# Performance work log

Hardware: AMD Instinct MI355X
Metric: run time of the kernel (lower is better)

The kernel has to match this reference:

```python
import jax, jax.numpy as jnp
import numpy as np

B, S, H, E, V, T = 64, 256, 1024, 512, 10000, 64
D = H // 2  # per-direction LSTM hidden


def setup_inputs() -> dict:
    key = jax.random.key(0)
    ks = jax.random.split(key, 16)
    s = jnp.float32(0.02)
    emb = jax.random.normal(ks[4], (V, E), jnp.float32) * s
    emb = emb.at[0].set(0.0)  # padding_idx=0
    return {
        "encoder_outputs": jax.random.normal(ks[0], (B, S, H), jnp.float32),
        "enc_h0": jax.random.normal(ks[1], (2, B, D), jnp.float32),
        "enc_c0": jax.random.normal(ks[2], (2, B, D), jnp.float32),
        "target": jax.random.randint(ks[3], (B, T), 1, V),
        "mask": jnp.zeros((B, S), jnp.bool_),
        "sos_idx": 1,
        "emb": emb,
        "Wa": jax.random.normal(ks[5], (H, H), jnp.float32) * s,
        "Ua": jax.random.normal(ks[6], (H, H), jnp.float32) * s,
        "Va": jax.random.normal(ks[7], (H,), jnp.float32) * s,
        "out_W": jax.random.normal(ks[8], (V, H), jnp.float32) * s,
        "out_b": jnp.zeros((V,), jnp.float32),
        "Wih_f": jax.random.normal(ks[9], (4 * D, E + H), jnp.float32) * s,
        "Whh_f": jax.random.normal(ks[10], (4 * D, D), jnp.float32) * s,
        "bih_f": jnp.zeros((4 * D,), jnp.float32),
        "bhh_f": jnp.zeros((4 * D,), jnp.float32),
        "Wih_b": jax.random.normal(ks[11], (4 * D, E + H), jnp.float32) * s,
        "Whh_b": jax.random.normal(ks[12], (4 * D, D), jnp.float32) * s,
        "bih_b": jnp.zeros((4 * D,), jnp.float32),
        "bhh_b": jnp.zeros((4 * D,), jnp.float32),
    }


def _lstm_cell(x, h, c, Wih, Whh, bih, bhh):
    g = x @ Wih.T + h @ Whh.T + bih + bhh
    i, f, gg, o = jnp.split(g, 4, axis=-1)  # torch gate order i,f,g,o
    c2 = jax.nn.sigmoid(f) * c + jax.nn.sigmoid(i) * jnp.tanh(gg)
    h2 = jax.nn.sigmoid(o) * jnp.tanh(c2)
    return h2, c2


def reference(encoder_outputs, enc_h0, enc_c0, target, mask, sos_idx, emb, Wa, Ua, Va,
              out_W, out_b, Wih_f, Whh_f, bih_f, bhh_f, Wih_b, Whh_b, bih_b, bhh_b):
    # Cache Ua(keys) once (original recomputes it each step; math identical).
    Uk = jnp.einsum('bsh,kh->bsk', encoder_outputs, Ua)  # [B,S,H]
    b = encoder_outputs.shape[0]
    tokens = jnp.concatenate(
        [jnp.full((b, 1), sos_idx, target.dtype), target[:, :-1]], axis=1)  # [B,T]
    xs = tokens.T  # [T,B]

    def step(carry, tok):
        h, c = carry  # each [2,B,D]
        query = jnp.swapaxes(h, 0, 1).reshape(b, -1)  # [B,H] (fwd||bwd)
        sc = jnp.einsum('bsh,h->bs', jnp.tanh((query @ Wa.T)[:, None, :] + Uk), Va)
        sc = jnp.where(mask, -jnp.inf, sc)
        w = jax.nn.softmax(sc, axis=-1)  # [B,S]
        ctx = jnp.einsum('bs,bsh->bh', w, encoder_outputs)  # [B,H]
        x = jnp.concatenate([emb[tok], ctx], axis=-1)  # [B,E+H]
        hf, cf = _lstm_cell(x, h[0], c[0], Wih_f, Whh_f, bih_f, bhh_f)
        hb, cb = _lstm_cell(x, h[1], c[1], Wih_b, Whh_b, bih_b, bhh_b)
        out = jnp.concatenate([hf, hb], axis=-1)  # [B,H]
        logits = out @ out_W.T + out_b  # [B,V]
        return (jnp.stack([hf, hb]), jnp.stack([cf, cb])), (logits, w)

    (h, c), (logits, attns) = jax.lax.scan(step, (enc_h0, enc_c0), xs)
    decoder_outputs = jnp.swapaxes(logits, 0, 1)  # [B,T,V]
    attentions = jnp.swapaxes(attns, 0, 1)        # [B,T,S]
    return decoder_outputs, h, c, attentions
```

## Files before the change

kernel.cpp:

```cpp
#include <hip/hip_runtime.h>

#define NB 64
#define NS 256
#define NH 1024
#define NE 512
#define NV 10000
#define NT 64
#define ND 512
#define NEH 1536
#define HST (65 * NH)

typedef __attribute__((ext_vector_type(8))) short bf16x8;
typedef __attribute__((ext_vector_type(4))) float f32x4;

__device__ __forceinline__ short F2B(float f) {
  unsigned u = __float_as_uint(f);
  return (short)((u + 0x7fffu + ((u >> 16) & 1u)) >> 16);
}
__device__ __forceinline__ float B2F(short s) {
  return __uint_as_float(((unsigned)(unsigned short)s) << 16);
}
__device__ __forceinline__ float ftanh(float x) {
  float e = __expf(2.f * x);
  return 1.f - 2.f * __builtin_amdgcn_rcpf(e + 1.f);
}

#define GLD16(src, dst)                                                        \
  __builtin_amdgcn_global_load_lds(                                            \
      (const __attribute__((address_space(1))) void*)(src),                    \
      (__attribute__((address_space(3))) void*)(dst), 16, 0, 0)

__device__ __forceinline__ void mm64_f32a(
    const float* __restrict__ Af, int lda, const short* __restrict__ Wg,
    int ldw, int K, short* Ch, size_t ldc, char* smem)
{
  const int tid = threadIdx.x;
  const int lane = tid & 63, w = tid >> 6;
  const int qm = (w >> 1) << 5, qn = (w & 1) << 5;
  const int kg = lane >> 4, rl = lane & 15;
  f32x4 acc[2][2] = {};
  const int nIt = K >> 6;

  auto stage = [&](int k0, int buf) {
    char* As = smem + (buf << 14);
    char* Bs = As + 8192;
#pragma unroll
    for (int p = 0; p < 2; ++p) {
      int j = tid + (p << 8);
      int row = j >> 3;
      int c = (j & 7) ^ (row & 7);
      const float* src = Af + (size_t)row * lda + k0 + (c << 3);
      float4 v0 = ((const float4*)src)[0];
      float4 v1 = ((const float4*)src)[1];
      bf16x8 pk;
      pk[0] = F2B(v0.x); pk[1] = F2B(v0.y); pk[2] = F2B(v0.z); pk[3] = F2B(v0.w);
      pk[4] = F2B(v1.x); pk[5] = F2B(v1.y); pk[6] = F2B(v1.z); pk[7] = F2B(v1.w);
      *((bf16x8*)As + j) = pk;
    }
#pragma unroll
    for (int p = 0; p < 2; ++p) {
      int j = (w << 7) + (p << 6) + lane;
      int row = j >> 3;
      int c = (j & 7) ^ (row & 7);
      GLD16(Wg + (size_t)row * ldw + k0 + (c << 3), Bs + (w << 11) + (p << 10));
    }
  };

  stage(0, 0);
  for (int it = 0; it < nIt; ++it) {
    __syncthreads();
    if (it + 1 < nIt) stage((it + 1) << 6, (it + 1) & 1);
    const short* As = (const short*)(smem + ((it & 1) << 14));
    const short* Bs = As + 4096;
#pragma unroll
    for (int kk = 0; kk < 2; ++kk) {
      bf16x8 af[2], bfr[2];
#pragma unroll
      for (int mt = 0; mt < 2; ++mt) {
        int r2 = qm + (mt << 4) + rl;
        int c = (kk << 2) + kg;
        af[mt] = *((const bf16x8*)As + ((r2 << 3) | (c ^ (r2 & 7))));
      }
#pragma unroll
      for (int nt = 0; nt < 2; ++nt) {
        int r2 = qn + (nt << 4) + rl;
        int c = (kk << 2) + kg;
        bfr[nt] = *((const bf16x8*)Bs + ((r2 << 3) | (c ^ (r2 & 7))));
      }
#pragma unroll
      for (int mt = 0; mt < 2; ++mt)
#pragma unroll
        for (int nt = 0; nt < 2; ++nt)
          acc[mt][nt] = __builtin_amdgcn_mfma_f32_16x16x32_bf16(
              af[mt], bfr[nt], acc[mt][nt], 0, 0, 0);
    }
  }
#pragma unroll
  for (int mt = 0; mt < 2; ++mt)
#pragma unroll
    for (int nt = 0; nt < 2; ++nt) {
      int cn = qn + (nt << 4) + rl;
#pragma unroll
      for (int r = 0; r < 4; ++r) {
        int rowm = qm + (mt << 4) + (kg << 2) + r;
        Ch[(size_t)rowm * ldc + cn] = F2B(acc[mt][nt][r]);
      }
    }
}

__global__ __launch_bounds__(256) void uk_mm_f32(const float* __restrict__ enc,
                                                 const short* __restrict__ Ua_h,
                                                 short* __restrict__ Uk_h) {
  __shared__ char smem[32768];
  mm64_f32a(enc + (size_t)blockIdx.y * 64 * NH, NH,
            Ua_h + (size_t)blockIdx.x * 64 * NH, NH, NH,
            Uk_h + (size_t)blockIdx.y * 64 * NH + blockIdx.x * 64, NH, smem);
}

template <int MODE>
__global__ __launch_bounds__(256) void mm128p(
    const short* __restrict__ A, const short* __restrict__ Bw, int nvmax,
    const float* __restrict__ bias, float* __restrict__ Cf,
    short* __restrict__ Ch)
{
  __shared__ char smem[65536];
  const int tid = threadIdx.x, lane = tid & 63, w = tid >> 6;
  const int m0 = blockIdx.x << 7;
  const int n0 = blockIdx.y << 7;
  const int qm = (w >> 1) << 6, qn = (w & 1) << 6;
  const int kg = lane >> 4, rl = lane & 15;
  f32x4 acc[4][4] = {};

  auto stage = [&](int it, int buf) {
    char* dst = smem + (buf << 15);
    const int k0 = it << 6;
#pragma unroll
    for (int p = 0; p < 4; ++p) {
      int j = (((w << 2) + p) << 6) + lane;
      int row = j >> 3;
      int c = (j & 7) ^ (row & 7);
      int m = m0 + row;
      size_t arow = (MODE == 0) ? ((size_t)(m >> 6) * 65 + (m & 63) + 1)
                                : (size_t)m;
      GLD16(A + arow * NH + k0 + (c << 3), dst + (((w << 2) + p) << 10));
      int vr = n0 + row; if (vr > nvmax - 1) vr = nvmax - 1;
      GLD16(Bw + (size_t)vr * NH + k0 + (c << 3),
            dst + 16384 + (((w << 2) + p) << 10));
    }
  };

  stage(0, 0); stage(1, 1);
  for (int it = 0; it < 16; ++it) {
    if (it < 15) asm volatile("s_waitcnt vmcnt(8)" ::: "memory");
    else         asm volatile("s_waitcnt vmcnt(0)" ::: "memory");
    __builtin_amdgcn_s_barrier();
    __builtin_amdgcn_sched_barrier(0);
    const short* As = (const short*)(smem + ((it & 1) << 15));
    const short* Bs = As + 8192;
#pragma unroll
    for (int kk = 0; kk < 2; ++kk) {
      bf16x8 af[4], bfr[4];
#pragma unroll
      for (int mt = 0; mt < 4; ++mt) {
        int r2 = qm + (mt << 4) + rl;
        int c = (kk << 2) + kg;
        af[mt] = *((const bf16x8*)As + ((r2 << 3) | (c ^ (r2 & 7))));
      }
#pragma unroll
      for (int nt = 0; nt < 4; ++nt) {
        int r2 = qn + (nt << 4) + rl;
        int c = (kk << 2) + kg;
        bfr[nt] = *((const bf16x8*)Bs + ((r2 << 3) | (c ^ (r2 & 7))));
      }
#pragma unroll
      for (int mt = 0; mt < 4; ++mt)
#pragma unroll
        for (int nt = 0; nt < 4; ++nt)
          acc[mt][nt] = __builtin_amdgcn_mfma_f32_16x16x32_bf16(
              af[mt], bfr[nt], acc[mt][nt], 0, 0, 0);
    }
    __builtin_amdgcn_sched_barrier(0);
    __builtin_amdgcn_s_barrier();
    if (it + 2 < 16) stage(it + 2, it & 1);
  }
#pragma unroll
  for (int nt = 0; nt < 4; ++nt) {
    int colv = n0 + qn + (nt << 4) + rl;
    if (colv < nvmax) {
#pragma unroll
      for (int mt = 0; mt < 4; ++mt)
#pragma unroll
        for (int r = 0; r < 4; ++r) {
          int m = m0 + qm + (mt << 4) + (kg << 2) + r;
          if (MODE == 0) {
            Cf[(size_t)m * NV + colv] = acc[mt][nt][r] + bias[colv];
          } else {
            Ch[(size_t)m * NH + colv] = F2B(acc[mt][nt][r]);
          }
        }
    }
  }
}

__global__ __launch_bounds__(256) void gates_v2(
    const short* __restrict__ Xt, const short* __restrict__ hcur,
    const short* __restrict__ Wcomb, const float* __restrict__ bperm,
    const float* __restrict__ cq_old, float* __restrict__ hq_f,
    float* __restrict__ cq_new, short* __restrict__ hnext)
{
  __shared__ char smem[61440];
  const int tid = threadIdx.x, lane = tid & 63, w = tid >> 6;
  const int kg = lane >> 4, rl = lane & 15;
  const int dir = blockIdx.x >> 7, gi = blockIdx.x & 127;
  const int hoff = dir << 9;
  const short* Wbase = Wcomb + (((size_t)(dir << 11) + (gi << 4)) << 11);

  auto stage = [&](int it, int buf) {
    char* dst = smem + buf * 20480;
#pragma unroll
    for (int g = 0; g < 4; ++g) {
      int row = (g << 4) + (w << 2) + kg;
      int c = rl ^ (row & 15);
      int k = (it << 7) + (c << 3);
      const short* src = (k < NEH)
          ? (Xt + (size_t)row * NEH + k)
          : (hcur + (size_t)row * HST + hoff + (k - NEH));
      GLD16(src, dst + (g << 12) + (w << 10));
    }
    {
      int rowB = (w << 2) + kg;
      int cB = rl ^ rowB;
      int kB = (it << 7) + (cB << 3);
      GLD16(Wbase + (size_t)rowB * 2048 + kB, dst + 16384 + (w << 10));
    }
  };

  stage(0, 0); stage(1, 1); stage(2, 2);
  f32x4 acc = {};
  int buf = 0;
  for (int it = 0; it < 16; ++it) {
    if (it < 14)      asm volatile("s_waitcnt vmcnt(10)" ::: "memory");
    else if (it == 14) asm volatile("s_waitcnt vmcnt(5)" ::: "memory");
    else               asm volatile("s_waitcnt vmcnt(0)" ::: "memory");
    __builtin_amdgcn_s_barrier();
    __builtin_amdgcn_sched_barrier(0);
    const short* As = (const short*)(smem + buf * 20480);
    const short* Bs = (const short*)(smem + buf * 20480 + 16384);
    const int rowA = (w << 4) + rl;
#pragma unroll
    for (int kk = 0; kk < 4; ++kk) {
      int chunk = (kk << 2) | kg;
      bf16x8 af = *((const bf16x8*)As + ((rowA << 4) | (chunk ^ (rowA & 15))));
      bf16x8 bf = *((const bf16x8*)Bs + ((rl << 4) | (chunk ^ rl)));
      acc = __builtin_amdgcn_mfma_f32_16x16x32_bf16(af, bf, acc, 0, 0, 0);
    }
    __builtin_amdgcn_sched_barrier(0);
    __builtin_amdgcn_s_barrier();
    if (it + 3 < 16) stage(it + 3, buf);
    buf = (buf == 2) ? 0 : buf + 1;
  }
  float* gacc = (float*)smem;
#pragma unroll
  for (int r = 0; r < 4; ++r)
    gacc[((w << 4) + (kg << 2) + r) * 17 + rl] = acc[r];
  __syncthreads();
  {
    const int b = tid >> 2, j2 = tid & 3;
    const float* bp = bperm + (dir << 11) + (gi << 4) + (j2 << 2);
    const float* gr = gacc + b * 17 + (j2 << 2);
    float gi_ = gr[0] + bp[0];
    float gf_ = gr[1] + bp[1];
    float gg_ = gr[2] + bp[2];
    float go_ = gr[3] + bp[3];
    const int d = ((gi >> 2) << 4) + (((gi << 2) + j2) & 15);
    const int idx = (b << 10) + hoff + d;
    float c0v = cq_old[idx];
    float si = 1.f / (1.f + __expf(-gi_));
    float sf = 1.f / (1.f + __expf(-gf_));
    float so = 1.f / (1.f + __expf(-go_));
    float tg = ftanh(gg_);
    float c2 = sf * c0v + si * tg;
    float h2 = so * ftanh(c2);
    hq_f[idx] = h2;
    cq_new[idx] = c2;
    hnext[(size_t)b * HST + hoff + d] = F2B(h2);
  }
}

__global__ __launch_bounds__(256) void q_mm2(const short* __restrict__ hcur,
                                             const short* __restrict__ Wa_h,
                                             float* __restrict__ q)
{
  __shared__ char smem[61440];
  const int tid = threadIdx.x, lane = tid & 63, w = tid >> 6;
  const int kg = lane >> 4, rl = lane & 15;
  const int n0 = blockIdx.x << 4;
  const short* Wbase = Wa_h + (size_t)n0 * NH;

  auto stage = [&](int it, int buf) {
    char* dst = smem + buf * 20480;
#pragma unroll
    for (int g = 0; g < 4; ++g) {
      int row = (g << 4) + (w << 2) + kg;
      int c = rl ^ (row & 15);
      int k = (it << 7) + (c << 3);
      GLD16(hcur + (size_t)row * HST + k, dst + (g << 12) + (w << 10));
    }
    {
      int rowB = (w << 2) + kg;
      int cB = rl ^ rowB;
      int kB = (it << 7) + (cB << 3);
      GLD16(Wbase + (size_t)rowB * NH + kB, dst + 16384 + (w << 10));
    }
  };

  stage(0, 0); stage(1, 1); stage(2, 2);
  f32x4 acc = {};
  int buf = 0;
  for (int it = 0; it < 8; ++it) {
    if (it < 6)       asm volatile("s_waitcnt vmcnt(10)" ::: "memory");
    else if (it == 6) asm volatile("s_waitcnt vmcnt(5)" ::: "memory");
    else              asm volatile("s_waitcnt vmcnt(0)" ::: "memory");
    __builtin_amdgcn_s_barrier();
    __builtin_amdgcn_sched_barrier(0);
    const short* As = (const short*)(smem + buf * 20480);
    const short* Bs = (const short*)(smem + buf * 20480 + 16384);
    const int rowA = (w << 4) + rl;
#pragma unroll
    for (int kk = 0; kk < 4; ++kk) {
      int chunk = (kk << 2) | kg;
      bf16x8 af = *((const bf16x8*)As + ((rowA << 4) | (chunk ^ (rowA & 15))));
      bf16x8 bf = *((const bf16x8*)Bs + ((rl << 4) | (chunk ^ rl)));
      acc = __builtin_amdgcn_mfma_f32_16x16x32_bf16(af, bf, acc, 0, 0, 0);
    }
    __builtin_amdgcn_sched_barrier(0);
    __builtin_amdgcn_s_barrier();
    if (it + 3 < 8) stage(it + 3, buf);
    buf = (buf == 2) ? 0 : buf + 1;
  }
#pragma unroll
  for (int r = 0; r < 4; ++r)
    q[(size_t)((w << 4) + (kg << 2) + r) * NH + n0 + rl] = acc[r];
}

__global__ __launch_bounds__(256) void f2b_k(const float* __restrict__ in,
                                             short* __restrict__ out, int n4) {
  int i = blockIdx.x * 256 + threadIdx.x;
  const int stride = gridDim.x * 256;
  for (; i < n4; i += stride) {
    float4 v = ((const float4*)in)[i];
    short4 o;
    o.x = F2B(v.x); o.y = F2B(v.y); o.z = F2B(v.z); o.w = F2B(v.w);
    ((short4*)out)[i] = o;
  }
}

__global__ __launch_bounds__(256) void f2b8_k(const float* __restrict__ in,
                                              short* __restrict__ outb,
                                              unsigned* __restrict__ out8,
                                              int n4) {
  int i = blockIdx.x * 256 + threadIdx.x;
  const int stride = gridDim.x * 256;
  for (; i < n4; i += stride) {
    float4 v = ((const float4*)in)[i];
    short4 o;
    o.x = F2B(v.x); o.y = F2B(v.y); o.z = F2B(v.z); o.w = F2B(v.w);
    ((short4*)outb)[i] = o;
    if (out8) {
      int u = __builtin_amdgcn_cvt_pk_fp8_f32(v.x, v.y, 0, false);
      u = __builtin_amdgcn_cvt_pk_fp8_f32(v.z, v.w, u, true);
      out8[i] = (unsigned)u;
    }
  }
}

__global__ __launch_bounds__(256) void f2b2_k(
    const float* __restrict__ in0, short* __restrict__ out0,
    const float* __restrict__ in1, short* __restrict__ out1, int n4each) {
  int i = blockIdx.x * 256 + threadIdx.x;
  const int stride = gridDim.x * 256;
  for (; i < 2 * n4each; i += stride) {
    const float* in = (i < n4each) ? in0 : in1;
    short* out = (i < n4each) ? out0 : out1;
    int j = (i < n4each) ? i : i - n4each;
    float4 v = ((const float4*)in)[j];
    short4 o;
    o.x = F2B(v.x); o.y = F2B(v.y); o.z = F2B(v.z); o.w = F2B(v.w);
    ((short4*)out)[j] = o;
  }
}

__global__ __launch_bounds__(256) void perm_w(
    const float* __restrict__ Wih_f, const float* __restrict__ Whh_f,
    const float* __restrict__ Wih_b, const float* __restrict__ Whh_b,
    const float* __restrict__ bih_f, const float* __restrict__ bhh_f,
    const float* __restrict__ bih_b, const float* __restrict__ bhh_b,
    short* __restrict__ Wcomb, float* __restrict__ bias_perm)
{
  int i = blockIdx.x * 256 + threadIdx.x;
  int k4 = i & 511;
  int np = (i >> 9) & 2047;
  int dir = i >> 20;
  int gate = np & 3, dlo = (np >> 2) & 15, dblk = np >> 6;
  int d = (dblk << 4) + dlo;
  int r = (gate << 9) + d;
  int k = k4 << 2;
  const float* Wih = dir ? Wih_b : Wih_f;
  const float* Whh = dir ? Whh_b : Whh_f;
  float4 v = (k < NEH) ? *(const float4*)(Wih + (size_t)r * NEH + k)
                       : *(const float4*)(Whh + (size_t)r * ND + (k - NEH));
  short4 o;
  o.x = F2B(v.x); o.y = F2B(v.y); o.z = F2B(v.z); o.w = F2B(v.w);
  *(short4*)(Wcomb + ((size_t)((dir << 11) + np) << 11) + k) = o;
  if (k4 == 0) {
    const float* bi = dir ? bih_b : bih_f;
    const float* bh = dir ? bhh_b : bhh_f;
    bias_perm[(dir << 11) + np] = bi[r] + bh[r];
  }
}

__global__ __launch_bounds__(256) void emb_fill(
    const float* __restrict__ emb, const int* __restrict__ target,
    const int* __restrict__ sos, short* __restrict__ Xbuf)
{
  int idx = blockIdx.x * 256 + threadIdx.x;
  int t = idx >> 13;
  int r = idx & 8191;
  int b = r >> 7, e4 = r & 127;
  int tok = (t == 0) ? sos[0] : target[b * NT + t - 1];
  float4 v = *(const float4*)(emb + (size_t)tok * NE + (e4 << 2));
  short4 o;
  o.x = F2B(v.x); o.y = F2B(v.y); o.z = F2B(v.z); o.w = F2B(v.w);
  *(short4*)(Xbuf + (size_t)(t * NB + b) * NEH + (e4 << 2)) = o;
}

__global__ __launch_bounds__(256) void init_state(
    const float* __restrict__ h0, const float* __restrict__ c0,
    float* __restrict__ hq, float* __restrict__ cq, short* __restrict__ H0) {
  int idx = blockIdx.x * 256 + threadIdx.x;
  int b = idx >> 10, dir = (idx >> 9) & 1, d = idx & 511;
  int src = dir * NB * ND + (b << 9) + d;
  float h = h0[src];
  hq[idx] = h;
  cq[idx] = c0[src];
  H0[(size_t)b * HST + (dir << 9) + d] = F2B(h);
}

__global__ __launch_bounds__(256) void final_state(
    const float* __restrict__ hq, const float* __restrict__ cq,
    float* __restrict__ out_h, float* __restrict__ out_c) {
  int idx = blockIdx.x * 256 + threadIdx.x;
  int dir = idx >> 15, r = idx & 32767, b = r >> 9, d = r & 511;
  int src = b * NH + dir * ND + d;
  out_h[idx] = hq[src];
  out_c[idx] = cq[src];
}

__global__ __launch_bounds__(256) void attn_score(
    const float* __restrict__ q, const short* __restrict__ Uk,
    const float* __restrict__ Va, const unsigned char* __restrict__ mask,
    float* __restrict__ sc) {
  __shared__ float qs[NH];
  const int b = blockIdx.x >> 6;
  {
    int t4 = threadIdx.x << 2;
    *(float4*)(qs + t4) = *(const float4*)(q + (size_t)b * NH + t4);
  }
  __syncthreads();
  const int lane = threadIdx.x & 63, wid = threadIdx.x >> 6;
  const int bs = (blockIdx.x << 2) + wid;
  const short* ukp = Uk + (size_t)bs * NH;
  float acc = 0.f;
#pragma unroll
  for (int i = 0; i < 2; ++i) {
    int h = (i << 9) + (lane << 3);
    bf16x8 uv = *(const bf16x8*)(ukp + h);
    float4 q0 = *(const float4*)(qs + h);
    float4 q1 = *(const float4*)(qs + h + 4);
    float4 v0 = *(const float4*)(Va + h);
    float4 v1 = *(const float4*)(Va + h + 4);
    acc += v0.x * ftanh(q0.x + B2F(uv[0]));
    acc += v0.y * ftanh(q0.y + B2F(uv[1]));
    acc += v0.z * ftanh(q0.z + B2F(uv[2]));
    acc += v0.w * ftanh(q0.w + B2F(uv[3]));
    acc += v1.x * ftanh(q1.x + B2F(uv[4]));
    acc += v1.y * ftanh(q1.y + B2F(uv[5]));
    acc += v1.z * ftanh(q1.z + B2F(uv[6]));
    acc += v1.w * ftanh(q1.w + B2F(uv[7]));
  }
#pragma unroll
  for (int o = 32; o; o >>= 1) acc += __shfl_down(acc, o);
  if (lane == 0) sc[bs] = mask[bs] ? -__builtin_inff() : acc;
}

__global__ __launch_bounds__(512) void ctx_soft(
    const float* __restrict__ sc, const unsigned char* __restrict__ enc8,
    const short* __restrict__ enc_h, const float* __restrict__ enc_f,
    int use_8, int use_h,
    short* __restrict__ Xt, float* __restrict__ attn_out, int t) {
  const int tid = threadIdx.x;
  const int b = blockIdx.x >> 2, qh = blockIdx.x & 3;
  __shared__ float red[8];
  __shared__ float ws[NS];
  __shared__ float4 red4[512];
  const int s8 = tid & 255;
  float v = sc[b * NS + s8];
  float m = v;
#pragma unroll
  for (int o = 32; o; o >>= 1) m = fmaxf(m, __shfl_down(m, o));
  if ((tid & 63) == 0) red[tid >> 6] = m;
  __syncthreads();
  m = fmaxf(fmaxf(fmaxf(red[0], red[1]), fmaxf(red[2], red[3])),
            fmaxf(fmaxf(red[4], red[5]), fmaxf(red[6], red[7])));
  float e = __expf(v - m);
  float su = e;
#pragma unroll
  for (int o = 32; o; o >>= 1) su += __shfl_down(su, o);
  __syncthreads();
  if ((tid & 63) == 0) red[tid >> 6] = su;
  __syncthreads();
  su = red[0] + red[1] + red[2] + red[3];
  float wgt = e / su;
  ws[s8] = wgt;
  if (qh == 0 && tid < 256) attn_out[((size_t)b * NT + t) * NS + tid] = wgt;
  __syncthreads();
  const int w8 = tid >> 6, l = tid & 63;
  const int h = (qh << 8) + (l << 2);
  const int s0 = w8 << 5;
  float4 a = make_float4(0.f, 0.f, 0.f, 0.f);
  if (use_8) {
    const unsigned char* ep = enc8 + ((size_t)b * NS + s0) * NH + h;
#pragma unroll 4
    for (int s = 0; s < 32; ++s) {
      int u = *(const int*)(ep + (size_t)s * NH);
      float wv = ws[s0 + s];
      a.x += wv * __builtin_amdgcn_cvt_f32_fp8(u, 0);
      a.y += wv * __builtin_amdgcn_cvt_f32_fp8(u, 1);
      a.z += wv * __builtin_amdgcn_cvt_f32_fp8(u, 2);
      a.w += wv * __builtin_amdgcn_cvt_f32_fp8(u, 3);
    }
  } else if (use_h) {
    const short* ep = enc_h + ((size_t)b * NS + s0) * NH + h;
    for (int s = 0; s < 32; ++s) {
      short4 vv = *(const short4*)(ep + (size_t)s * NH);
      float wv = ws[s0 + s];
      a.x += wv * B2F(vv.x); a.y += wv * B2F(vv.y);
      a.z += wv * B2F(vv.z); a.w += wv * B2F(vv.w);
    }
  } else {
    const float* ep = enc_f + ((size_t)b * NS + s0) * NH + h;
    for (int s = 0; s < 32; ++s) {
      float4 vv = *(const float4*)(ep + (size_t)s * NH);
      float wv = ws[s0 + s];
      a.x += wv * vv.x; a.y += wv * vv.y; a.z += wv * vv.z; a.w += wv * vv.w;
    }
  }
  red4[(w8 << 6) + l] = a;
  __syncthreads();
  if (tid < 64) {
    float sx = 0.f, sy = 0.f, sz = 0.f, sw = 0.f;
#pragma unroll
    for (int k = 0; k < 8; ++k) {
      float4 r = red4[(k << 6) + tid];
      sx += r.x; sy += r.y; sz += r.z; sw += r.w;
    }
    short4 o;
    o.x = F2B(sx); o.y = F2B(sy); o.z = F2B(sz); o.w = F2B(sw);
    *(short4*)(Xt + (size_t)b * NEH + NE + (qh << 8) + (tid << 2)) = o;
  }
}

extern "C" void kernel_launch(void* const* d_in, const int* in_sizes, int n_in,
                              void* d_out, int out_size, void* d_ws, size_t ws_size,
                              hipStream_t stream)
{
  const float* enc    = (const float*)d_in[0];
  const float* h0     = (const float*)d_in[1];
  const float* c0     = (const float*)d_in[2];
  const int*   target = (const int*)d_in[3];
  const unsigned char* mask = (const unsigned char*)d_in[4];
  const int*   sos    = (const int*)d_in[5];
  const float* emb    = (const float*)d_in[6];
  const float* Wa     = (const float*)d_in[7];
  const float* Ua     = (const float*)d_in[8];
  const float* Va     = (const float*)d_in[9];
  const float* out_W  = (const float*)d_in[10];
  const float* out_b  = (const float*)d_in[11];
  const float* Wih_f  = (const float*)d_in[12];
  const float* Whh_f  = (const float*)d_in[13];
  const float* bih_f  = (const float*)d_in[14];
  const float* bhh_f  = (const float*)d_in[15];
  const float* Wih_b  = (const float*)d_in[16];
  const float* Whh_b  = (const float*)d_in[17];
  const float* bih_b  = (const float*)d_in[18];
  const float* bhh_b  = (const float*)d_in[19];

  float* out_dec  = (float*)d_out;
  float* out_h    = out_dec + (size_t)NB * NT * NV;
  float* out_c    = out_h + 2 * NB * ND;
  float* out_attn = out_c + 2 * NB * ND;

  char* base = (char*)d_ws;
  size_t off = 0;
  auto alloc = [&](size_t bytes) -> char* {
    char* p = base + off;
    off += (bytes + 255) & ~(size_t)255;
    return p;
  };
  short* Uk_h  = (short*)alloc((size_t)NB * NS * NH * 2);
  short* ow_h  = (short*)alloc((size_t)NV * NH * 2);
  short* Ua_h  = (short*)alloc((size_t)NH * NH * 2);
  short* Wa_h  = (short*)alloc((size_t)NH * NH * 2);
  short* Wcomb = (short*)alloc((size_t)2 * 2048 * 2048 * 2);
  float* bperm = (float*)alloc((size_t)2 * 2048 * 4);
  float* q     = (float*)alloc((size_t)NB * NH * 4);
  float* sc    = (float*)alloc((size_t)NB * NS * 4);
  short* Xbuf  = (short*)alloc((size_t)NT * NB * NEH * 2);
  float* hq    = (float*)alloc((size_t)NB * NH * 4);
  float* cq    = (float*)alloc((size_t)2 * NB * NH * 4);
  short* Hbuf  = (short*)alloc((size_t)NB * HST * 2);
  short* enc_h = nullptr;
  unsigned char* enc8 = nullptr;
  int use_h = 0, use_8 = 0;
  if (off + (size_t)NB * NS * NH * 2 <= ws_size) {
    enc_h = (short*)alloc((size_t)NB * NS * NH * 2);
    use_h = 1;
    if (off + (size_t)NB * NS * NH <= ws_size) {
      enc8 = (unsigned char*)alloc((size_t)NB * NS * NH);
      use_8 = 1;
    }
  }
  if (off > ws_size) return;

  f2b_k<<<dim3(2048), dim3(256), 0, stream>>>(out_W, ow_h, NV * NH / 4);
  f2b2_k<<<dim3(2048), dim3(256), 0, stream>>>(Ua, Ua_h, Wa, Wa_h, NH * NH / 4);
  perm_w<<<dim3(8192), dim3(256), 0, stream>>>(Wih_f, Whh_f, Wih_b, Whh_b,
                                               bih_f, bhh_f, bih_b, bhh_b,
                                               Wcomb, bperm);
  emb_fill<<<dim3(2048), dim3(256), 0, stream>>>(emb, target, sos, Xbuf);
  init_state<<<dim3(256), dim3(256), 0, stream>>>(h0, c0, hq, cq, Hbuf);
  if (use_h) {
    f2b8_k<<<dim3(2048), dim3(256), 0, stream>>>(enc, enc_h, (unsigned*)enc8,
                                                 NB * NS * NH / 4);
    mm128p<1><<<dim3(128, 8), dim3(256), 0, stream>>>(enc_h, Ua_h, NH, nullptr,
                                                      nullptr, Uk_h);
  } else {
    uk_mm_f32<<<dim3(16, 256), dim3(256), 0, stream>>>(enc, Ua_h, Uk_h);
  }

  for (int t = 0; t < NT; ++t) {
    const short* hcur = Hbuf + (size_t)t * NH;
    short* hnext = Hbuf + (size_t)(t + 1) * NH;
    float* cq_cur = cq + (t & 1) * (NB * NH);
    float* cq_nxt = cq + ((t & 1) ^ 1) * (NB * NH);
    short* Xt = Xbuf + (size_t)t * NB * NEH;

    q_mm2<<<dim3(64), dim3(256), 0, stream>>>(hcur, Wa_h, q);
    attn_score<<<dim3(4096), dim3(256), 0, stream>>>(q, Uk_h, Va, mask, sc);
    ctx_soft<<<dim3(256), dim3(512), 0, stream>>>(sc, enc8, enc_h, enc,
                                                  use_8, use_h,
                                                  Xt, out_attn, t);
    gates_v2<<<dim3(256), dim3(256), 0, stream>>>(Xt, hcur, Wcomb, bperm,
                                                  cq_cur, hq, cq_nxt, hnext);
  }

  mm128p<0><<<dim3(32, 79), dim3(256), 0, stream>>>(Hbuf, ow_h, NV,
                                                    out_b, out_dec, nullptr);
  final_state<<<dim3(256), dim3(256), 0, stream>>>(hq, cq, out_h, out_c);
}
```

Before: 1.972 ms.

## Precompute embedding contribution to LSTM gates for all timesteps in one GEMM

Adds a batched GEMM that multiplies every timestep's token embeddings by the embedding slice of the gate weights before the recurrent loop, storing bf16 gate partials. The per-step gates kernel then skips the first 512 K columns (12 instead of 16 iterations) and adds the precomputed partial in its epilogue. This moves a quarter of the serial per-step gate GEMM work off the recurrence critical path, at the cost of an extra workspace buffer, an up-front GEMM, and bf16 rounding of the embedding partial sums.

Result: faster. 1.842 ms (-6.6%).

```diff
diff --git a/kernel.cpp b/kernel.cpp
--- a/kernel.cpp
+++ b/kernel.cpp
@@ -202,11 +202,87 @@
   }
 }
 
+__global__ __launch_bounds__(256) void emb_mm(
+    const short* __restrict__ A, const short* __restrict__ Bw,
+    short* __restrict__ Ch)
+{
+  __shared__ char smem[65536];
+  const int tid = threadIdx.x, lane = tid & 63, w = tid >> 6;
+  const int m0 = blockIdx.x << 7;
+  const int n0 = blockIdx.y << 7;
+  const int qm = (w >> 1) << 6, qn = (w & 1) << 6;
+  const int kg = lane >> 4, rl = lane & 15;
+  f32x4 acc[4][4] = {};
+
+  auto stage = [&](int it, int buf) {
+    char* dst = smem + (buf << 15);
+    const int k0 = it << 6;
+#pragma unroll
+    for (int p = 0; p < 4; ++p) {
+      int j = (((w << 2) + p) << 6) + lane;
+      int row = j >> 3;
+      int c = (j & 7) ^ (row & 7);
+      GLD16(A + (size_t)(m0 + row) * NEH + k0 + (c << 3),
+            dst + (((w << 2) + p) << 10));
+      GLD16(Bw + (size_t)(n0 + row) * 2048 + k0 + (c << 3),
+            dst + 16384 + (((w << 2) + p) << 10));
+    }
+  };
+
+  stage(0, 0); stage(1, 1);
+  for (int it = 0; it < 8; ++it) {
+    if (it < 7) asm volatile("s_waitcnt vmcnt(8)" ::: "memory");
+    else        asm volatile("s_waitcnt vmcnt(0)" ::: "memory");
+    __builtin_amdgcn_s_barrier();
+    __builtin_amdgcn_sched_barrier(0);
+    const short* As = (const short*)(smem + ((it & 1) << 15));
+    const short* Bs = As + 8192;
+#pragma unroll
+    for (int kk = 0; kk < 2; ++kk) {
+      bf16x8 af[4], bfr[4];
+#pragma unroll
+      for (int mt = 0; mt < 4; ++mt) {
+        int r2 = qm + (mt << 4) + rl;
+        int c = (kk << 2) + kg;
+        af[mt] = *((const bf16x8*)As + ((r2 << 3) | (c ^ (r2 & 7))));
+      }
+#pragma unroll
+      for (int nt = 0; nt < 4; ++nt) {
+        int r2 = qn + (nt << 4) + rl;
+        int c = (kk << 2) + kg;
+        bfr[nt] = *((const bf16x8*)Bs + ((r2 << 3) | (c ^ (r2 & 7))));
+      }
+#pragma unroll
+      for (int mt = 0; mt < 4; ++mt)
+#pragma unroll
+        for (int nt = 0; nt < 4; ++nt)
+          acc[mt][nt] = __builtin_amdgcn_mfma_f32_16x16x32_bf16(
+              af[mt], bfr[nt], acc[mt][nt], 0, 0, 0);
+    }
+    __builtin_amdgcn_sched_barrier(0);
+    __builtin_amdgcn_s_barrier();
+    if (it + 2 < 8) stage(it + 2, it & 1);
+  }
+#pragma unroll
+  for (int nt = 0; nt < 4; ++nt) {
+    int colv = n0 + qn + (nt << 4) + rl;
+#pragma unroll
+    for (int mt = 0; mt < 4; ++mt)
+#pragma unroll
+      for (int r = 0; r < 4; ++r) {
+        int m = m0 + qm + (mt << 4) + (kg << 2) + r;
+        Ch[(size_t)m * 4096 + colv] = F2B(acc[mt][nt][r]);
+      }
+  }
+}
+
+template <int USEG>
 __global__ __launch_bounds__(256) void gates_v2(
     const short* __restrict__ Xt, const short* __restrict__ hcur,
     const short* __restrict__ Wcomb, const float* __restrict__ bperm,
     const float* __restrict__ cq_old, float* __restrict__ hq_f,
-    float* __restrict__ cq_new, short* __restrict__ hnext)
+    float* __restrict__ cq_new, short* __restrict__ hnext,
+    const short* __restrict__ Gemb_t)
 {
   __shared__ char smem[61440];
   const int tid = threadIdx.x, lane = tid & 63, w = tid >> 6;
@@ -214,6 +290,10 @@
   const int dir = blockIdx.x >> 7, gi = blockIdx.x & 127;
   const int hoff = dir << 9;
   const short* Wbase = Wcomb + (((size_t)(dir << 11) + (gi << 4)) << 11);
+  const int NIT = USEG ? 12 : 16;
+  const int KB0 = USEG ? 512 : 0;
+  const int XOFF = USEG ? 512 : 0;
+  const int HBND = USEG ? 1024 : NEH;
 
   auto stage = [&](int it, int buf) {
     char* dst = smem + buf * 20480;
@@ -222,26 +302,26 @@
       int row = (g << 4) + (w << 2) + kg;
       int c = rl ^ (row & 15);
       int k = (it << 7) + (c << 3);
-      const short* src = (k < NEH)
-          ? (Xt + (size_t)row * NEH + k)
-          : (hcur + (size_t)row * HST + hoff + (k - NEH));
+      const short* src = (k < HBND)
+          ? (Xt + (size_t)row * NEH + XOFF + k)
+          : (hcur + (size_t)row * HST + hoff + (k - HBND));
       GLD16(src, dst + (g << 12) + (w << 10));
     }
     {
       int rowB = (w << 2) + kg;
       int cB = rl ^ rowB;
       int kB = (it << 7) + (cB << 3);
-      GLD16(Wbase + (size_t)rowB * 2048 + kB, dst + 16384 + (w << 10));
+      GLD16(Wbase + (size_t)rowB * 2048 + KB0 + kB, dst + 16384 + (w << 10));
     }
   };
 
   stage(0, 0); stage(1, 1); stage(2, 2);
   f32x4 acc = {};
   int buf = 0;
-  for (int it = 0; it < 16; ++it) {
-    if (it < 14)      asm volatile("s_waitcnt vmcnt(10)" ::: "memory");
-    else if (it == 14) asm volatile("s_waitcnt vmcnt(5)" ::: "memory");
-    else               asm volatile("s_waitcnt vmcnt(0)" ::: "memory");
+  for (int it = 0; it < NIT; ++it) {
+    if (it < NIT - 2)       asm volatile("s_waitcnt vmcnt(10)" ::: "memory");
+    else if (it == NIT - 2) asm volatile("s_waitcnt vmcnt(5)" ::: "memory");
+    else                    asm volatile("s_waitcnt vmcnt(0)" ::: "memory");
     __builtin_amdgcn_s_barrier();
     __builtin_amdgcn_sched_barrier(0);
     const short* As = (const short*)(smem + buf * 20480);
@@ -256,7 +336,7 @@
     }
     __builtin_amdgcn_sched_barrier(0);
     __builtin_amdgcn_s_barrier();
-    if (it + 3 < 16) stage(it + 3, buf);
+    if (it + 3 < NIT) stage(it + 3, buf);
     buf = (buf == 2) ? 0 : buf + 1;
   }
   float* gacc = (float*)smem;
@@ -272,6 +352,11 @@
     float gf_ = gr[1] + bp[1];
     float gg_ = gr[2] + bp[2];
     float go_ = gr[3] + bp[3];
+    if (USEG) {
+      short4 ge = *(const short4*)(Gemb_t + (size_t)b * 4096 + (dir << 11) +
+                                   (gi << 4) + (j2 << 2));
+      gi_ += B2F(ge.x); gf_ += B2F(ge.y); gg_ += B2F(ge.z); go_ += B2F(ge.w);
+    }
     const int d = ((gi >> 2) << 4) + (((gi << 2) + j2) & 15);
     const int idx = (b << 10) + hoff + d;
     float c0v = cq_old[idx];
@@ -621,13 +706,18 @@
   short* Hbuf  = (short*)alloc((size_t)NB * HST * 2);
   short* enc_h = nullptr;
   unsigned char* enc8 = nullptr;
-  int use_h = 0, use_8 = 0;
+  short* Gemb = nullptr;
+  int use_h = 0, use_8 = 0, use_g = 0;
   if (off + (size_t)NB * NS * NH * 2 <= ws_size) {
     enc_h = (short*)alloc((size_t)NB * NS * NH * 2);
     use_h = 1;
     if (off + (size_t)NB * NS * NH <= ws_size) {
       enc8 = (unsigned char*)alloc((size_t)NB * NS * NH);
       use_8 = 1;
+      if (off + (size_t)NT * NB * 4096 * 2 <= ws_size) {
+        Gemb = (short*)alloc((size_t)NT * NB * 4096 * 2);
+        use_g = 1;
+      }
     }
   }
   if (off > ws_size) return;
@@ -647,6 +737,8 @@
   } else {
     uk_mm_f32<<<dim3(16, 256), dim3(256), 0, stream>>>(enc, Ua_h, Uk_h);
   }
+  if (use_g)
+    emb_mm<<<dim3(32, 32), dim3(256), 0, stream>>>(Xbuf, Wcomb, Gemb);
 
   for (int t = 0; t < NT; ++t) {
     const short* hcur = Hbuf + (size_t)t * NH;
@@ -660,8 +752,13 @@
     ctx_soft<<<dim3(256), dim3(512), 0, stream>>>(sc, enc8, enc_h, enc,
                                                   use_8, use_h,
                                                   Xt, out_attn, t);
-    gates_v2<<<dim3(256), dim3(256), 0, stream>>>(Xt, hcur, Wcomb, bperm,
-                                                  cq_cur, hq, cq_nxt, hnext);
+    if (use_g)
+      gates_v2<1><<<dim3(256), dim3(256), 0, stream>>>(
+          Xt, hcur, Wcomb, bperm, cq_cur, hq, cq_nxt, hnext,
+          Gemb + (size_t)t * NB * 4096);
+    else
+      gates_v2<0><<<dim3(256), dim3(256), 0, stream>>>(
+          Xt, hcur, Wcomb, bperm, cq_cur, hq, cq_nxt, hnext, nullptr);
   }
 
   mm128p<0><<<dim3(32, 79), dim3(256), 0, stream>>>(Hbuf, ow_h, NV,
```
